# Optimization experiments

Hardware: AMD Instinct MI355X
Metric: run time of the kernel (lower is better)

Reference implementation:

```python
import jax, jax.numpy as jnp
import numpy as np

B, S, D, MULT, K, EPS = 8, 2048, 512, 4, 9, 1e-6


def setup_inputs() -> dict:
    key = jax.random.key(0)
    ks = jax.random.split(key, 12)
    w = lambda k, shape, s=0.02: jax.random.normal(k, shape, dtype=jnp.float32) * s
    return dict(
        x=jax.random.normal(ks[0], (B, S, D), dtype=jnp.float32),
        g=jnp.ones((D,), jnp.float32),
        W1=w(ks[1], (D, D)), b1=jnp.zeros((D,), jnp.float32),
        W2=w(ks[2], (D, D)), b2=jnp.zeros((D,), jnp.float32),
        dw_w=w(ks[3], (D, D, K)), dw_b=jnp.zeros((D,), jnp.float32),
        pw_w=w(ks[4], (D, D, 1)), pw_b=jnp.zeros((D,), jnp.float32),
        Wi=w(ks[5], (D, D)), bi=jnp.zeros((D,), jnp.float32),
        Wr=w(ks[6], (D, D)), br=jnp.zeros((D,), jnp.float32),
        lam=jax.random.normal(ks[7], (D,), dtype=jnp.float32),
        Wm1=w(ks[8], (D, D * MULT)), bm1=jnp.zeros((D * MULT,), jnp.float32),
        Wm2=w(ks[9], (D * MULT, D)), bm2=jnp.zeros((D,), jnp.float32),
    )


def _rglru(x, Wi, bi, Wr, br, lam):
    # Griffin RG-LRU: h_t = a_t * h_{t-1} + sqrt(1 - a_t^2) * (i_t * x_t), h_0 = 0
    r = jax.nn.sigmoid(x @ Wr + br)                 # [B,S,D] recurrence gate
    i = jax.nn.sigmoid(x @ Wi + bi)                 # [B,S,D] input gate
    log_a = -8.0 * jax.nn.softplus(lam) * r         # [B,S,D]
    a = jnp.exp(log_a)
    b = jnp.sqrt(1.0 - jnp.exp(2.0 * log_a)) * (i * x)

    def combine(e1, e2):
        a1, b1 = e1
        a2, b2 = e2
        return (a1 * a2, a2 * b1 + b2)

    _, h = jax.lax.associative_scan(combine, (a, b), axis=1)
    return h


def _conv1d(x_cdS, w_oik, b_o, pad):
    y = jax.lax.conv_general_dilated(
        x_cdS, w_oik, window_strides=(1,), padding=[pad],
        dimension_numbers=("NCH", "OIH", "NCH"))
    return y + b_o[None, :, None]


def reference(x, g, W1, b1, W2, b2, dw_w, dw_b, pw_w, pw_b,
              Wi, bi, Wr, br, lam, Wm1, bm1, Wm2, bm2):
    scale = jnp.sqrt(jnp.float32(D))

    def rms(t):  # matches torch: x / (||x||_2 + eps) * sqrt(D) * g
        n = jnp.linalg.norm(t, axis=-1, keepdims=True) + EPS
        return t / n * scale * g

    skip = x
    xn = rms(x)
    l1 = xn @ W1 + b1                               # [B,S,D]
    l2 = xn @ W2 + b2                               # [B,S,D]
    c = jnp.transpose(l1, (0, 2, 1))                # [B,D,S]
    c = _conv1d(c, dw_w, dw_b, (K // 2, K // 2))    # 'same' padding, k=9
    c = _conv1d(c, pw_w, pw_b, (0, 0))              # pointwise k=1
    l1 = jnp.transpose(c, (0, 2, 1))                # [B,S,D]
    l1 = _rglru(l1, Wi, bi, Wr, br, lam)
    x1 = l1 * jax.nn.gelu(l2, approximate=False) + skip

    skip2 = x1
    xn2 = rms(x1)
    h = xn2 @ Wm1 + bm1                             # [B,S,4D]
    out = (jax.nn.gelu(h, approximate=False) * h) @ Wm2 + bm2 + skip2
    return out
```

## Files before the change

kernel.cpp:

```cpp
#include <hip/hip_runtime.h>
#include <hip/hip_bf16.h>

typedef unsigned short ushort_t;
typedef unsigned short vus8 __attribute__((ext_vector_type(8)));
typedef short vs8 __attribute__((ext_vector_type(8)));
typedef float vf4 __attribute__((ext_vector_type(4)));

#define D_DIM 512
#define S_LEN 2048
#define B_SZ 8
#define T_TOK 16384
#define NCH 64
#define CLEN 32

__device__ __forceinline__ float bf2f(ushort_t u) {
  union { unsigned int i; float f; } v;
  v.i = ((unsigned int)u) << 16;
  return v.f;
}
__device__ __forceinline__ ushort_t f2bf(float f) {
  union { float f; unsigned int i; } v;
  v.f = f;
  unsigned int r = v.i + 0x7fffu + ((v.i >> 16) & 1u);
  return (ushort_t)(r >> 16);
}
__device__ __forceinline__ float gelu_exact(float x) {
  return 0.5f * x * (1.0f + erff(x * 0.7071067811865475f));
}
__device__ __forceinline__ float ld_in(const void* p, size_t i, int fl) {
  return fl ? ((const float*)p)[i] : bf2f(((const ushort_t*)p)[i]);
}
__device__ __forceinline__ int dt_fl(const ushort_t* gdt) {
  return !(gdt[0] == 0x3F80 && gdt[1] == 0x3F80);
}
__device__ __forceinline__ void gld_lds16(const ushort_t* g, ushort_t* l) {
  __builtin_amdgcn_global_load_lds(
      (const __attribute__((address_space(1))) unsigned int*)g,
      (__attribute__((address_space(3))) unsigned int*)l, 16, 0, 0);
}

__device__ __forceinline__ void ab_compute(ushort_t rp, ushort_t ip, ushort_t xv,
                                           float sp8, float& a, float& b) {
  float r = 1.f / (1.f + expf(-bf2f(rp)));
  float ig = 1.f / (1.f + expf(-bf2f(ip)));
  float la = -sp8 * r;
  a = expf(la);
  b = sqrtf(fmaxf(0.f, -expm1f(2.f * la))) * ig * bf2f(xv);
}

#define NJOBS 18
struct PrepJobs {
  const void* src[NJOBS];
  ushort_t* dst[NJOBS];
  int R[NJOBS];
  int C[NJOBS];
  int mode[NJOBS];
  int start[NJOBS];
  const void* gsrc;
  int njobs;
};
__global__ void mega_prep(PrepJobs J, const ushort_t* __restrict__ gdt) {
  __shared__ ushort_t ts[32][33];
  int fl = dt_fl(gdt);
  int bid = blockIdx.x;
  int j = 0;
  while (j + 1 < J.njobs && bid >= J.start[j + 1]) j++;
  int tile = bid - J.start[j];
  const void* in = J.src[j];
  ushort_t* out = J.dst[j];
  int mode = J.mode[j];
  if (mode == 2) {
    int n = J.R[j];
    int base = tile * 8192;
#pragma unroll 4
    for (int q = 0; q < 32; q++) {
      int i = base + q * 256 + threadIdx.x;
      if (i < n) out[i] = fl ? f2bf(((const float*)in)[i]) : ((const ushort_t*)in)[i];
    }
    return;
  }
  int R = J.R[j], C = J.C[j];
  int tpr = C >> 5;
  int bc = tile % tpr, br = tile / tpr;
  int tx = threadIdx.x & 31, ty = threadIdx.x >> 5;
#pragma unroll
  for (int i = 0; i < 32; i += 8) {
    size_t idx = (size_t)(br * 32 + ty + i) * C + bc * 32 + tx;
    ts[ty + i][tx] = fl ? f2bf(((const float*)in)[idx]) : ((const ushort_t*)in)[idx];
  }
  __syncthreads();
#pragma unroll
  for (int i = 0; i < 32; i += 8) {
    int r = bc * 32 + ty + i;
    int orow = (mode == 1) ? (r % 9) * 512 + r / 9 : r;
    ushort_t val = ts[tx][ty + i];
    if (mode == 3) {
      int kcol = br * 32 + tx;
      val = f2bf(bf2f(val) * ld_in(J.gsrc, kcol, fl));
    }
    out[(size_t)orow * R + br * 32 + tx] = val;
  }
}

__global__ void gam_kernel(const ushort_t* __restrict__ tpw, const ushort_t* __restrict__ dwbc,
                           const ushort_t* __restrict__ pwbc, const ushort_t* __restrict__ lamc,
                           float* __restrict__ gam, float* __restrict__ sp8b) {
  int t = blockIdx.x * 256 + threadIdx.x;
  if (t < 512) {
    float l = bf2f(lamc[t]);
    sp8b[t] = 8.f * ((l > 20.f) ? l : log1pf(expf(l)));
  }
  int wave = threadIdx.x >> 6, lane = threadIdx.x & 63;
  int o = blockIdx.x * 4 + wave;
  vus8 v = *(const vus8*)(tpw + (size_t)o * 512 + lane * 8);
  vus8 w = *(const vus8*)(dwbc + lane * 8);
  float p = 0.f;
#pragma unroll
  for (int q = 0; q < 8; q++) p += bf2f(v[q]) * bf2f(w[q]);
#pragma unroll
  for (int off = 32; off; off >>= 1) p += __shfl_xor(p, off, 64);
  if (lane == 0) gam[o] = p + bf2f(pwbc[o]);
}

__global__ void rms_kernel(const void* __restrict__ x, const ushort_t* __restrict__ gdt,
                           const ushort_t* __restrict__ gc, ushort_t* __restrict__ out) {
  int fl = dt_fl(gdt);
  int wave = threadIdx.x >> 6, lane = threadIdx.x & 63;
  int row = blockIdx.x * 4 + wave;
  size_t base = (size_t)row * D_DIM + lane * 8;
  float f[8];
  float ss = 0.f;
#pragma unroll
  for (int j = 0; j < 8; j++) { f[j] = ld_in(x, base + j, fl); ss += f[j] * f[j]; }
#pragma unroll
  for (int off = 32; off > 0; off >>= 1) ss += __shfl_xor(ss, off, 64);
  float sc = 22.62741699796952f / (sqrtf(ss) + 1e-6f);
  vus8 o;
#pragma unroll
  for (int j = 0; j < 8; j++) o[j] = f2bf(f[j] * sc * bf2f(gc[lane * 8 + j]));
  *(vus8*)(out + base) = o;
}

template <int ACT>
__global__ __launch_bounds__(256, 2) void gemm_bt(
    const ushort_t* __restrict__ A, const ushort_t* __restrict__ Bt,
    const ushort_t* __restrict__ bias, void* __restrict__ Cv,
    const ushort_t* __restrict__ skip, const float* __restrict__ rowss,
    const ushort_t* __restrict__ gdt, int N, int K, int lda, int row0,
    size_t zsA, size_t zsB, size_t zsC) {
  __shared__ __align__(16) ushort_t As[128 * 32];
  __shared__ __align__(16) ushort_t Bs[128 * 32];
  A += (size_t)blockIdx.z * zsA;
  Bt += (size_t)blockIdx.z * zsB;
  const size_t zC = (size_t)blockIdx.z * zsC;
  const int tid = threadIdx.x;
  const int bm = blockIdx.y, bn = blockIdx.x;
  const int wave = tid >> 6, lane = tid & 63;
  const int wm = wave & 1, wn = wave >> 1;
  const int quad = lane >> 4, l16 = lane & 15;
  const int ofl = (ACT == 2) ? dt_fl(gdt) : 0;
  const int srow = wave * 32 + (lane >> 2);
  const int scol = (lane & 3) * 8;
  const ushort_t* gA = A + (size_t)(bm * 128 + srow) * lda + scol;
  const ushort_t* gB = Bt + (size_t)(bn * 128 + srow) * K + scol;
  ushort_t* lA0 = As + (wave * 32) * 32;
  ushort_t* lA1 = As + (wave * 32 + 16) * 32;
  ushort_t* lB0 = Bs + (wave * 32) * 32;
  ushort_t* lB1 = Bs + (wave * 32 + 16) * 32;
  vf4 acc[4][4] = {};
  for (int k0 = 0; k0 < K; k0 += 32) {
    __syncthreads();
    gld_lds16(gA + k0, lA0);
    gld_lds16(gA + k0 + (size_t)16 * lda, lA1);
    gld_lds16(gB + k0, lB0);
    gld_lds16(gB + k0 + (size_t)16 * K, lB1);
    __syncthreads();
    vs8 af[4], bfr[4];
#pragma unroll
    for (int mi = 0; mi < 4; mi++)
      af[mi] = *(const vs8*)(As + (wm * 64 + mi * 16 + l16) * 32 + quad * 8);
#pragma unroll
    for (int ni = 0; ni < 4; ni++)
      bfr[ni] = *(const vs8*)(Bs + (wn * 64 + ni * 16 + l16) * 32 + quad * 8);
#pragma unroll
    for (int mi = 0; mi < 4; mi++)
#pragma unroll
      for (int ni = 0; ni < 4; ni++)
        acc[mi][ni] =
            __builtin_amdgcn_mfma_f32_16x16x32_bf16(af[mi], bfr[ni], acc[mi][ni], 0, 0, 0);
  }
#pragma unroll
  for (int mi = 0; mi < 4; mi++) {
#pragma unroll
    for (int ni = 0; ni < 4; ni++) {
      int gcol = bn * 128 + wn * 64 + ni * 16 + l16;
      float bv = bias ? bf2f(bias[gcol]) : 0.f;
#pragma unroll
      for (int r = 0; r < 4; r++) {
        int grow = row0 + bm * 128 + wm * 64 + mi * 16 + quad * 4 + r;
        size_t oidx = zC + (size_t)grow * N + gcol;
        float v;
        if (ACT == 3) {
          float sc = 22.62741699796952f / (sqrtf(rowss[grow]) + 1e-6f);
          v = acc[mi][ni][r] * sc + bv;
          v = gelu_exact(v) * v;
        } else {
          v = acc[mi][ni][r] + bv;
        }
        if (ACT == 2) v += bf2f(skip[(size_t)grow * N + gcol]);
        if (ACT == 2 && ofl) ((float*)Cv)[oidx] = v;
        else ((ushort_t*)Cv)[oidx] = f2bf(v);
      }
    }
  }
}

template <int ACT>
__global__ __launch_bounds__(512, 2) void gemm256(
    const ushort_t* __restrict__ A, const ushort_t* __restrict__ Bt,
    const ushort_t* __restrict__ bias, ushort_t* __restrict__ C,
    const float* __restrict__ rowss, int N, int K) {
  __shared__ __align__(16) ushort_t lds[65536];
  const int tid = threadIdx.x;
  const int bn = blockIdx.x, bm = blockIdx.y;
  const int wave = tid >> 6, lane = tid & 63;
  const int wm = wave & 1, wn = wave >> 1;
  const int quad = lane >> 4, l16 = lane & 15;
  const int NT = K >> 5;

  const int r2 = tid >> 2;
  const int scol = (((tid & 3) ^ ((r2 >> 1) & 3)) << 3);
  const ushort_t* gA0 = A + (size_t)(bm * 256 + r2) * K + scol;
  const ushort_t* gB0 = Bt + (size_t)(bn * 256 + r2) * K + scol;
  const size_t hstep = (size_t)128 * K;
  ushort_t* ldsW = lds + (wave << 9);

  const int cA = ((quad ^ ((l16 >> 1) & 3)) << 3);

  vf4 acc[8][4] = {};

#define STAGE(t, slot)                            \
  do {                                            \
    const ushort_t* ga = gA0 + (t) * 32;          \
    const ushort_t* gb = gB0 + (t) * 32;          \
    ushort_t* d = ldsW + (slot) * 16384;          \
    gld_lds16(ga, d);                             \
    gld_lds16(ga + hstep, d + 4096);              \
    gld_lds16(gb, d + 8192);                      \
    gld_lds16(gb + hstep, d + 12288);             \
  } while (0)

  STAGE(0, 0);
  STAGE(1, 1);

  for (int t = 0; t < NT; ++t) {
    if (t + 1 < NT)
      asm volatile("s_waitcnt vmcnt(4)" ::: "memory");
    else
      asm volatile("s_waitcnt vmcnt(0)" ::: "memory");
    __builtin_amdgcn_s_barrier();
    __builtin_amdgcn_sched_barrier(0);
    if (t + 2 < NT) STAGE(t + 2, (t + 2) & 3);
    const ushort_t* L = lds + (t & 3) * 16384;
    vs8 af[8], bf[4];
#pragma unroll
    for (int mi = 0; mi < 8; mi++)
      af[mi] = *(const vs8*)(L + (wm * 128 + mi * 16 + l16) * 32 + cA);
#pragma unroll
    for (int ni = 0; ni < 4; ni++)
      bf[ni] = *(const vs8*)(L + 8192 + (wn * 64 + ni * 16 + l16) * 32 + cA);
    asm volatile("s_waitcnt lgkmcnt(0)" ::: "memory");
    __builtin_amdgcn_sched_barrier(0);
    __builtin_amdgcn_s_setprio(1);
#pragma unroll
    for (int mi = 0; mi < 8; mi++)
#pragma unroll
      for (int ni = 0; ni < 4; ni++)
        acc[mi][ni] =
            __builtin_amdgcn_mfma_f32_16x16x32_bf16(af[mi], bf[ni], acc[mi][ni], 0, 0, 0);
    __builtin_amdgcn_s_setprio(0);
    __builtin_amdgcn_sched_barrier(0);
  }
#undef STAGE

#pragma unroll
  for (int mi = 0; mi < 8; mi++) {
    const int growb = bm * 256 + wm * 128 + mi * 16 + quad * 4;
    float scv[4];
    if (ACT == 3) {
#pragma unroll
      for (int r = 0; r < 4; r++)
        scv[r] = 22.62741699796952f / (sqrtf(rowss[growb + r]) + 1e-6f);
    }
#pragma unroll
    for (int ni = 0; ni < 4; ni++) {
      const int gcol = bn * 256 + wn * 64 + ni * 16 + l16;
      const float bv = bf2f(bias[gcol]);
#pragma unroll
      for (int r = 0; r < 4; r++) {
        float v = acc[mi][ni][r];
        if (ACT == 3) {
          v = v * scv[r] + bv;
          v = gelu_exact(v) * v;
        } else {
          v += bv;
        }
        C[(size_t)(growb + r) * N + gcol] = f2bf(v);
      }
    }
  }
}

#define LDA_CONV 1024
__global__ __launch_bounds__(256, 2) void conv_gemm(
    const ushort_t* __restrict__ A, const ushort_t* __restrict__ Bt9,
    const float* __restrict__ gam, ushort_t* __restrict__ C) {
  __shared__ __align__(16) ushort_t Ah[136 * 32];
  __shared__ __align__(16) ushort_t Bs[3 * 128 * 32];
  const int tid = threadIdx.x;
  const int bid = blockIdx.x;
  const int xid = bid & 7, cid = bid >> 3;
  const int bn = xid >> 1;
  const int bm = (xid & 1) * 64 + cid;
  const int wave = tid >> 6, lane = tid & 63;
  const int wm = wave & 1, wn = wave >> 1;
  const int quad = lane >> 4, l16 = lane & 15;
  const int pos = bm & 15;
  const bool first = (pos == 0), last = (pos == 15);
  const int blrow = lane >> 2;
  const int bscol = (lane & 3) * 8;
  vf4 acc[4][4] = {};
  for (int k0 = 0; k0 < D_DIM; k0 += 32) {
    __syncthreads();
    for (int c = tid; c < 544; c += 256) {
      int j = c >> 2, col = (c & 3) * 8;
      vus8 v = {0, 0, 0, 0, 0, 0, 0, 0};
      bool valid = !((first && j < 4) || (last && j >= 132));
      if (valid)
        v = *(const vus8*)(A + (size_t)(bm * 128 + j - 4) * LDA_CONV + k0 + col);
      *(vus8*)(Ah + j * 32 + col) = v;
    }
#pragma unroll
    for (int kg = 0; kg < 3; kg++) {
      if (kg) __syncthreads();
#pragma unroll
      for (int h = 0; h < 6; h++) {
        int m = h * 4 + wave;
        int r = m * 16 + blrow;
        int kbl = m >> 3;
        int ro = r & 127;
        const ushort_t* g = Bt9 + ((size_t)(kg * 3 + kbl) * D_DIM + bn * 128 + ro) * D_DIM +
                            k0 + bscol;
        gld_lds16(g, Bs + m * 16 * 32);
      }
      __syncthreads();
#pragma unroll
      for (int kbl = 0; kbl < 3; kbl++) {
        int kb = kg * 3 + kbl;
        vs8 af[4], bfr[4];
#pragma unroll
        for (int mi = 0; mi < 4; mi++)
          af[mi] = *(const vs8*)(Ah + (wm * 64 + mi * 16 + l16 + kb) * 32 + quad * 8);
#pragma unroll
        for (int ni = 0; ni < 4; ni++)
          bfr[ni] = *(const vs8*)(Bs + kbl * 4096 + (wn * 64 + ni * 16 + l16) * 32 + quad * 8);
#pragma unroll
        for (int mi = 0; mi < 4; mi++)
#pragma unroll
          for (int ni = 0; ni < 4; ni++)
            acc[mi][ni] =
                __builtin_amdgcn_mfma_f32_16x16x32_bf16(af[mi], bfr[ni], acc[mi][ni], 0, 0, 0);
      }
    }
  }
#pragma unroll
  for (int mi = 0; mi < 4; mi++) {
#pragma unroll
    for (int ni = 0; ni < 4; ni++) {
      int gcol = bn * 128 + wn * 64 + ni * 16 + l16;
      float gv = gam[gcol];
#pragma unroll
      for (int r = 0; r < 4; r++) {
        int grow = bm * 128 + wm * 64 + mi * 16 + quad * 4 + r;
        C[(size_t)grow * D_DIM + gcol] = f2bf(acc[mi][ni][r] + gv);
      }
    }
  }
}

__global__ void scan_pass1(const ushort_t* __restrict__ P, const ushort_t* __restrict__ xin,
                           const float* __restrict__ sp8b, float* __restrict__ Aagg,
                           float* __restrict__ Bagg) {
  int bid = blockIdx.x;
  int dblk = bid & 1, c = (bid >> 1) & (NCH - 1), bb = bid >> 7;
  int d = dblk * 256 + threadIdx.x;
  float sp8 = sp8b[d];
  size_t baseP = ((size_t)bb * S_LEN + c * CLEN) * 1024 + d;
  size_t baseX = ((size_t)bb * S_LEN + c * CLEN) * D_DIM + d;
  float Ap = 1.f, h = 0.f;
  for (int s = 0; s < CLEN; s++) {
    float av, bv;
    ab_compute(P[baseP + (size_t)s * 1024], P[baseP + 512 + (size_t)s * 1024],
               xin[baseX + (size_t)s * D_DIM], sp8, av, bv);
    Ap *= av;
    h = av * h + bv;
  }
  size_t o = ((size_t)bb * NCH + c) * D_DIM + d;
  Aagg[o] = Ap;
  Bagg[o] = h;
}

__global__ void scan_carry(const float* __restrict__ Aagg, const float* __restrict__ Bagg,
                           float* __restrict__ carry) {
  int idx = blockIdx.x * 256 + threadIdx.x;
  int bb = idx >> 9, d = idx & (D_DIM - 1);
  float h = 0.f;
  for (int c = 0; c < NCH; c++) {
    size_t o = ((size_t)bb * NCH + c) * D_DIM + d;
    carry[o] = h;
    h = Aagg[o] * h + Bagg[o];
  }
}

__global__ void scan_pass2(const ushort_t* __restrict__ P, const float* __restrict__ sp8b,
                           const float* __restrict__ carry, const ushort_t* __restrict__ P12,
                           const void* __restrict__ x, const ushort_t* __restrict__ gdt,
                           ushort_t* xio, float* __restrict__ rowss) {
  int fl = dt_fl(gdt);
  int bid = blockIdx.x;
  int dblk = bid & 1, c = (bid >> 1) & (NCH - 1), bb = bid >> 7;
  int d = dblk * 256 + threadIdx.x;
  int lane = threadIdx.x & 63;
  float sp8 = sp8b[d];
  float h = carry[((size_t)bb * NCH + c) * D_DIM + d];
  size_t baseP = ((size_t)bb * S_LEN + c * CLEN) * 1024 + d;
  size_t baseL = ((size_t)bb * S_LEN + c * CLEN) * 1024 + 512 + d;
  size_t base = ((size_t)bb * S_LEN + c * CLEN) * D_DIM + d;
  int row0 = bb * S_LEN + c * CLEN;
  for (int s = 0; s < CLEN; s++) {
    size_t idx = base + (size_t)s * D_DIM;
    float av, bv;
    ab_compute(P[baseP + (size_t)s * 1024], P[baseP + 512 + (size_t)s * 1024], xio[idx], sp8,
               av, bv);
    h = av * h + bv;
    float l2v = bf2f(P12[baseL + (size_t)s * 1024]);
    float xv = ld_in(x, idx, fl);
    float v = h * gelu_exact(l2v) + xv;
    xio[idx] = f2bf(v);
    float p = v * v;
#pragma unroll
    for (int o2 = 32; o2; o2 >>= 1) p += __shfl_xor(p, o2, 64);
    if (lane == 0) atomicAdd(&rowss[row0 + s], p);
  }
}

extern "C" void kernel_launch(void* const* d_in, const int* in_sizes, int n_in, void* d_out,
                              int out_size, void* d_ws, size_t ws_size, hipStream_t stream) {
  (void)in_sizes; (void)n_in; (void)out_size; (void)ws_size;
  const void* x   = d_in[0];
  const void* g   = d_in[1];
  const void* W1  = d_in[2];
  const void* b1  = d_in[3];
  const void* W2  = d_in[4];
  const void* b2  = d_in[5];
  const void* dww = d_in[6];
  const void* dwb = d_in[7];
  const void* pww = d_in[8];
  const void* pwb = d_in[9];
  const void* Wi  = d_in[10];
  const void* bi  = d_in[11];
  const void* Wr  = d_in[12];
  const void* br  = d_in[13];
  const void* lam = d_in[14];
  const void* Wm1 = d_in[15];
  const void* bm1 = d_in[16];
  const void* Wm2 = d_in[17];
  const void* bm2 = d_in[18];
  const ushort_t* gdt = (const ushort_t*)g;

  char* ws = (char*)d_ws;
  size_t off = 0;
  auto take = [&](size_t n) {
    void* p = ws + off;
    off += (n + 255) & ~(size_t)255;
    return p;
  };
  const size_t ACT_B = (size_t)T_TOK * D_DIM * 2;
  ushort_t* tW12 = (ushort_t*)take((size_t)1024 * 512 * 2);
  ushort_t* tWri = (ushort_t*)take((size_t)1024 * 512 * 2);
  ushort_t* tWm1 = (ushort_t*)take((size_t)2048 * 512 * 2);
  ushort_t* tWm2 = (ushort_t*)take((size_t)2048 * 512 * 2);
  ushort_t* Wp   = (ushort_t*)take((size_t)9 * 512 * 512 * 2);
  ushort_t* gc   = (ushort_t*)take(512 * 2);
  ushort_t* lamc = (ushort_t*)take(512 * 2);
  ushort_t* b12c = (ushort_t*)take(1024 * 2);
  ushort_t* bric = (ushort_t*)take(1024 * 2);
  ushort_t* bm2c = (ushort_t*)take(512 * 2);
  ushort_t* bm1c = (ushort_t*)take(2048 * 2);
  ushort_t* dwbc = (ushort_t*)take(512 * 2);
  ushort_t* pwbc = (ushort_t*)take(512 * 2);
  float* gam     = (float*)take(512 * 4);
  float* sp8b    = (float*)take(512 * 4);
  float* rowss   = (float*)take((size_t)T_TOK * 4);
  ushort_t* S0 = (ushort_t*)take(ACT_B);
  ushort_t* S1 = (ushort_t*)take(ACT_B);
  ushort_t* S2 = (ushort_t*)take(ACT_B);
  ushort_t* S3 = (ushort_t*)take(ACT_B);
  ushort_t* S4 = (ushort_t*)take(ACT_B);
  float* Aagg  = (float*)take((size_t)B_SZ * NCH * D_DIM * 4);
  float* Bagg  = (float*)take((size_t)B_SZ * NCH * D_DIM * 4);
  float* carry = (float*)take((size_t)B_SZ * NCH * D_DIM * 4);
  ushort_t* tpw  = S0;
  ushort_t* tdwT = S1;
  ushort_t* Pri  = S0;
  ushort_t* P12  = S2;
  ushort_t* u    = S0;

  hipMemsetAsync(rowss, 0, (size_t)T_TOK * 4, stream);

  PrepJobs J;
  const void* js[NJOBS] = {g, lam, b1, b2, dwb, pwb, br, bi, bm2, bm1, pww,
                           W1, W2, Wr, Wi, Wm1, Wm2, dww};
  ushort_t* jd[NJOBS] = {gc, lamc, b12c, b12c + 512, dwbc, pwbc, bric, bric + 512, bm2c, bm1c,
                         tpw, tW12, tW12 + (size_t)512 * 512, tWri, tWri + (size_t)512 * 512,
                         tWm1, tWm2, tdwT};
  int jR[NJOBS] = {512, 512, 512, 512, 512, 512, 512, 512, 512, 2048, 262144,
                   512, 512, 512, 512, 512, 2048, 512};
  int jC[NJOBS] = {0, 0, 0, 0, 0, 0, 0, 0, 0, 0, 0, 512, 512, 512, 512, 2048, 512, 4608};
  int jm[NJOBS] = {2, 2, 2, 2, 2, 2, 2, 2, 2, 2, 2, 0, 0, 0, 0, 3, 0, 1};
  int cum = 0;
  for (int i = 0; i < NJOBS; i++) {
    J.src[i] = js[i]; J.dst[i] = jd[i]; J.R[i] = jR[i]; J.C[i] = jC[i]; J.mode[i] = jm[i];
    J.start[i] = cum;
    cum += (jm[i] == 2) ? (jR[i] + 8191) / 8192 : (jC[i] / 32) * (jR[i] / 32);
  }
  J.gsrc = g;
  J.njobs = NJOBS;
  mega_prep<<<cum, 256, 0, stream>>>(J, gdt);
  gemm_bt<0><<<dim3(4, 4, 9), 256, 0, stream>>>(tpw, tdwT, nullptr, Wp, nullptr, nullptr, gdt,
                                                512, 512, 512, 0, 0, (size_t)512 * 512,
                                                (size_t)512 * 512);
  gam_kernel<<<128, 256, 0, stream>>>(tpw, dwbc, pwbc, lamc, gam, sp8b);

  rms_kernel<<<T_TOK / 4, 256, 0, stream>>>(x, gdt, gc, S4);
  gemm256<0><<<dim3(4, 64), 512, 0, stream>>>(S4, tW12, b12c, P12, nullptr, 1024, 512);
  conv_gemm<<<512, 256, 0, stream>>>(P12, Wp, gam, S4);
  gemm256<0><<<dim3(4, 64), 512, 0, stream>>>(S4, tWri, bric, Pri, nullptr, 1024, 512);
  scan_pass1<<<B_SZ * NCH * 2, 256, 0, stream>>>(Pri, S4, sp8b, Aagg, Bagg);
  scan_carry<<<16, 256, 0, stream>>>(Aagg, Bagg, carry);
  scan_pass2<<<B_SZ * NCH * 2, 256, 0, stream>>>(Pri, sp8b, carry, P12, x, gdt, S4, rowss);

  gemm256<3><<<dim3(8, 64), 512, 0, stream>>>(S4, tWm1, bm1c, u, rowss, 2048, 512);
  gemm_bt<2><<<dim3(4, 128), 256, 0, stream>>>(u, tWm2, bm2c, d_out, S4, nullptr, gdt, 512,
                                               2048, 2048, 0, 0, 0, 0);
}
```

Baseline: 509.5 us.

## Rewrite conv GEMM as pipelined 256-row kernel over zero-padded activation buffer

The W1/W2 GEMM now writes its output into a buffer that has 16 zero-padded rows per batch, so the depthwise+pointwise conv GEMM can read halo rows without boundary checks. Zeroing of the pad rows is added to the prep kernel. The conv kernel is replaced by a 512-thread, 256-row-tile version that software-pipelines global-to-LDS async loads of A (double buffered) and B (4 slots) across the 9 taps. It uses swizzled LDS layouts, explicit waitcnt and barriers, and raised priority around the MFMA blocks. The aim is to hide load latency and cut LDS bank conflicts, at the cost of fragile hand-tuned waitcnt counts and more LDS per block.

New measurement: 526.9 us. 3.4% more time.

```diff
diff --git a/kernel.cpp b/kernel.cpp
--- a/kernel.cpp
+++ b/kernel.cpp
@@ -12,6 +12,7 @@
 #define T_TOK 16384
 #define NCH 64
 #define CLEN 32
+#define APAD_ROWS 16640
 
 __device__ __forceinline__ float bf2f(ushort_t u) {
   union { unsigned int i; float f; } v;
@@ -48,7 +49,7 @@
   b = sqrtf(fmaxf(0.f, -expm1f(2.f * la))) * ig * bf2f(xv);
 }
 
-#define NJOBS 18
+#define NJOBS 27
 struct PrepJobs {
   const void* src[NJOBS];
   ushort_t* dst[NJOBS];
@@ -69,13 +70,15 @@
   const void* in = J.src[j];
   ushort_t* out = J.dst[j];
   int mode = J.mode[j];
-  if (mode == 2) {
+  if (mode == 2 || mode == 4) {
     int n = J.R[j];
     int base = tile * 8192;
 #pragma unroll 4
     for (int q = 0; q < 32; q++) {
       int i = base + q * 256 + threadIdx.x;
-      if (i < n) out[i] = fl ? f2bf(((const float*)in)[i]) : ((const ushort_t*)in)[i];
+      if (i < n)
+        out[i] = (mode == 4) ? (ushort_t)0
+                             : (fl ? f2bf(((const float*)in)[i]) : ((const ushort_t*)in)[i]);
     }
     return;
   }
@@ -305,83 +308,116 @@
         } else {
           v += bv;
         }
-        C[(size_t)(growb + r) * N + gcol] = f2bf(v);
+        int grow = growb + r;
+        size_t orow = (ACT == 1) ? (size_t)grow + (size_t)((grow >> 11) << 4) + 4
+                                 : (size_t)grow;
+        C[orow * N + gcol] = f2bf(v);
       }
     }
   }
 }
 
-#define LDA_CONV 1024
-__global__ __launch_bounds__(256, 2) void conv_gemm(
-    const ushort_t* __restrict__ A, const ushort_t* __restrict__ Bt9,
+__global__ __launch_bounds__(512, 2) void conv256(
+    const ushort_t* __restrict__ Apad, const ushort_t* __restrict__ Wp,
     const float* __restrict__ gam, ushort_t* __restrict__ C) {
-  __shared__ __align__(16) ushort_t Ah[136 * 32];
-  __shared__ __align__(16) ushort_t Bs[3 * 128 * 32];
+  __shared__ __align__(16) ushort_t Asl[2 * 12288];
+  __shared__ __align__(16) ushort_t Bsl[4 * 4096];
   const int tid = threadIdx.x;
-  const int bid = blockIdx.x;
-  const int xid = bid & 7, cid = bid >> 3;
-  const int bn = xid >> 1;
-  const int bm = (xid & 1) * 64 + cid;
+  const int bn = blockIdx.x;
+  const int bmg = blockIdx.y;
+  const int batch = bmg >> 3, seg = bmg & 7;
   const int wave = tid >> 6, lane = tid & 63;
-  const int wm = wave & 1, wn = wave >> 1;
+  const int wm = wave >> 1, wn = wave & 1;
   const int quad = lane >> 4, l16 = lane & 15;
-  const int pos = bm & 15;
-  const bool first = (pos == 0), last = (pos == 15);
-  const int blrow = lane >> 2;
-  const int bscol = (lane & 3) * 8;
+  const int r2 = tid >> 2;
+  const int sw0 = (((tid & 3) ^ ((r2 >> 1) & 3)) << 3);
+  const int cB = ((quad ^ ((l16 >> 1) & 3)) << 3);
+  const int bnc = bn * 128;
+  const size_t tb = (size_t)batch * 2064 + seg * 256;
+  const ushort_t* A0 = Apad + tb * 1024;
+
   vf4 acc[4][4] = {};
-  for (int k0 = 0; k0 < D_DIM; k0 += 32) {
-    __syncthreads();
-    for (int c = tid; c < 544; c += 256) {
-      int j = c >> 2, col = (c & 3) * 8;
-      vus8 v = {0, 0, 0, 0, 0, 0, 0, 0};
-      bool valid = !((first && j < 4) || (last && j >= 132));
-      if (valid)
-        v = *(const vus8*)(A + (size_t)(bm * 128 + j - 4) * LDA_CONV + k0 + col);
-      *(vus8*)(Ah + j * 32 + col) = v;
-    }
-#pragma unroll
-    for (int kg = 0; kg < 3; kg++) {
-      if (kg) __syncthreads();
-#pragma unroll
-      for (int h = 0; h < 6; h++) {
-        int m = h * 4 + wave;
-        int r = m * 16 + blrow;
-        int kbl = m >> 3;
-        int ro = r & 127;
-        const ushort_t* g = Bt9 + ((size_t)(kg * 3 + kbl) * D_DIM + bn * 128 + ro) * D_DIM +
-                            k0 + bscol;
-        gld_lds16(g, Bs + m * 16 * 32);
-      }
-      __syncthreads();
-#pragma unroll
-      for (int kbl = 0; kbl < 3; kbl++) {
-        int kb = kg * 3 + kbl;
-        vs8 af[4], bfr[4];
-#pragma unroll
-        for (int mi = 0; mi < 4; mi++)
-          af[mi] = *(const vs8*)(Ah + (wm * 64 + mi * 16 + l16 + kb) * 32 + quad * 8);
-#pragma unroll
-        for (int ni = 0; ni < 4; ni++)
-          bfr[ni] = *(const vs8*)(Bs + kbl * 4096 + (wn * 64 + ni * 16 + l16) * 32 + quad * 8);
-#pragma unroll
-        for (int mi = 0; mi < 4; mi++)
-#pragma unroll
-          for (int ni = 0; ni < 4; ni++)
-            acc[mi][ni] =
-                __builtin_amdgcn_mfma_f32_16x16x32_bf16(af[mi], bfr[ni], acc[mi][ni], 0, 0, 0);
-      }
-    }
-  }
+
+  auto stageA = [&](int tt, int slot, int part) {
+    gld_lds16(A0 + (size_t)(part * 128 + r2) * 1024 + tt * 32 + sw0,
+              Asl + slot * 12288 + part * 4096 + wave * 512);
+  };
+  auto stageB = [&](int tt, int pp, int slot) {
+    gld_lds16(Wp + (size_t)(pp * 512 + bnc + r2) * 512 + tt * 32 + sw0,
+              Bsl + slot * 4096 + wave * 512);
+  };
+
+#define CPHASE(T, P, NSTR, DO_A, DO_B)                                            \
+  do {                                                                            \
+    asm volatile("s_waitcnt " NSTR ::: "memory");                                 \
+    __builtin_amdgcn_s_barrier();                                                 \
+    __builtin_amdgcn_sched_barrier(0);                                            \
+    if (DO_A) stageA((T) + 1, ((T) + 1) & 1, (P));                                \
+    if (DO_B) {                                                                   \
+      int pp = (P) + 2, tt = (T);                                                 \
+      if (pp >= 9) { pp -= 9; tt++; }                                             \
+      stageB(tt, pp, ((T) * 9 + (P) + 2) & 3);                                    \
+    }                                                                             \
+    const ushort_t* LA = Asl + ((T) & 1) * 12288;                                 \
+    const ushort_t* LB = Bsl + (((T) * 9 + (P)) & 3) * 4096;                      \
+    vs8 af[4], bfv[4];                                                            \
+    _Pragma("unroll") for (int mi = 0; mi < 4; mi++) {                            \
+      int row = wm * 64 + mi * 16 + l16 + (P);                                    \
+      af[mi] = *(const vs8*)(LA + row * 32 + ((quad ^ ((row >> 1) & 3)) << 3));   \
+    }                                                                             \
+    _Pragma("unroll") for (int ni = 0; ni < 4; ni++)                              \
+      bfv[ni] = *(const vs8*)(LB + (wn * 64 + ni * 16 + l16) * 32 + cB);          \
+    asm volatile("s_waitcnt lgkmcnt(0)" ::: "memory");                            \
+    __builtin_amdgcn_sched_barrier(0);                                            \
+    __builtin_amdgcn_s_setprio(1);                                                \
+    _Pragma("unroll") for (int mi = 0; mi < 4; mi++)                              \
+      _Pragma("unroll") for (int ni = 0; ni < 4; ni++)                            \
+        acc[mi][ni] = __builtin_amdgcn_mfma_f32_16x16x32_bf16(af[mi], bfv[ni],    \
+                                                              acc[mi][ni], 0, 0, 0); \
+    __builtin_amdgcn_s_setprio(0);                                                \
+    __builtin_amdgcn_sched_barrier(0);                                            \
+  } while (0)
+
+  stageA(0, 0, 0);
+  stageA(0, 0, 1);
+  stageA(0, 0, 2);
+  stageB(0, 0, 0);
+  stageB(0, 1, 1);
+
+  for (int t = 0; t < 15; ++t) {
+    CPHASE(t, 0, "vmcnt(1)", 1, 1);
+    CPHASE(t, 1, "vmcnt(2)", 1, 1);
+    CPHASE(t, 2, "vmcnt(2)", 1, 1);
+    CPHASE(t, 3, "vmcnt(2)", 0, 1);
+    CPHASE(t, 4, "vmcnt(1)", 0, 1);
+    CPHASE(t, 5, "vmcnt(1)", 0, 1);
+    CPHASE(t, 6, "vmcnt(1)", 0, 1);
+    CPHASE(t, 7, "vmcnt(1)", 0, 1);
+    CPHASE(t, 8, "vmcnt(1)", 0, 1);
+  }
+  {
+    const int t = 15;
+    CPHASE(t, 0, "vmcnt(0)", 0, 1);
+    CPHASE(t, 1, "vmcnt(0)", 0, 1);
+    CPHASE(t, 2, "vmcnt(0)", 0, 1);
+    CPHASE(t, 3, "vmcnt(0)", 0, 1);
+    CPHASE(t, 4, "vmcnt(0)", 0, 1);
+    CPHASE(t, 5, "vmcnt(0)", 0, 1);
+    CPHASE(t, 6, "vmcnt(0)", 0, 1);
+    CPHASE(t, 7, "vmcnt(0)", 0, 0);
+    CPHASE(t, 8, "vmcnt(0)", 0, 0);
+  }
+#undef CPHASE
+
 #pragma unroll
   for (int mi = 0; mi < 4; mi++) {
 #pragma unroll
     for (int ni = 0; ni < 4; ni++) {
-      int gcol = bn * 128 + wn * 64 + ni * 16 + l16;
+      int gcol = bnc + wn * 64 + ni * 16 + l16;
       float gv = gam[gcol];
 #pragma unroll
       for (int r = 0; r < 4; r++) {
-        int grow = bm * 128 + wm * 64 + mi * 16 + quad * 4 + r;
+        int grow = (batch << 11) + seg * 256 + wm * 64 + mi * 16 + quad * 4 + r;
         C[(size_t)grow * D_DIM + gcol] = f2bf(acc[mi][ni][r] + gv);
       }
     }
@@ -423,7 +459,7 @@
 }
 
 __global__ void scan_pass2(const ushort_t* __restrict__ P, const float* __restrict__ sp8b,
-                           const float* __restrict__ carry, const ushort_t* __restrict__ P12,
+                           const float* __restrict__ carry, const ushort_t* __restrict__ l2p,
                            const void* __restrict__ x, const ushort_t* __restrict__ gdt,
                            ushort_t* xio, float* __restrict__ rowss) {
   int fl = dt_fl(gdt);
@@ -434,7 +470,7 @@
   float sp8 = sp8b[d];
   float h = carry[((size_t)bb * NCH + c) * D_DIM + d];
   size_t baseP = ((size_t)bb * S_LEN + c * CLEN) * 1024 + d;
-  size_t baseL = ((size_t)bb * S_LEN + c * CLEN) * 1024 + 512 + d;
+  size_t baseL = ((size_t)bb * 2064 + 4 + c * CLEN) * 1024 + 512 + d;
   size_t base = ((size_t)bb * S_LEN + c * CLEN) * D_DIM + d;
   int row0 = bb * S_LEN + c * CLEN;
   for (int s = 0; s < CLEN; s++) {
@@ -443,7 +479,7 @@
     ab_compute(P[baseP + (size_t)s * 1024], P[baseP + 512 + (size_t)s * 1024], xio[idx], sp8,
                av, bv);
     h = av * h + bv;
-    float l2v = bf2f(P12[baseL + (size_t)s * 1024]);
+    float l2v = bf2f(l2p[baseL + (size_t)s * 1024]);
     float xv = ld_in(x, idx, fl);
     float v = h * gelu_exact(l2v) + xv;
     xio[idx] = f2bf(v);
@@ -502,37 +538,47 @@
   float* gam     = (float*)take(512 * 4);
   float* sp8b    = (float*)take(512 * 4);
   float* rowss   = (float*)take((size_t)T_TOK * 4);
-  ushort_t* S0 = (ushort_t*)take(ACT_B);
-  ushort_t* S1 = (ushort_t*)take(ACT_B);
-  ushort_t* S2 = (ushort_t*)take(ACT_B);
-  ushort_t* S3 = (ushort_t*)take(ACT_B);
-  ushort_t* S4 = (ushort_t*)take(ACT_B);
+  ushort_t* Apad2 = (ushort_t*)take((size_t)APAD_ROWS * 1024 * 2);
+  ushort_t* PriB  = (ushort_t*)take((size_t)T_TOK * 1024 * 2);
+  ushort_t* S4    = (ushort_t*)take(ACT_B);
   float* Aagg  = (float*)take((size_t)B_SZ * NCH * D_DIM * 4);
   float* Bagg  = (float*)take((size_t)B_SZ * NCH * D_DIM * 4);
   float* carry = (float*)take((size_t)B_SZ * NCH * D_DIM * 4);
-  ushort_t* tpw  = S0;
-  ushort_t* tdwT = S1;
-  ushort_t* Pri  = S0;
-  ushort_t* P12  = S2;
-  ushort_t* u    = S0;
+  ushort_t* tpw  = PriB;
+  ushort_t* tdwT = PriB + 262144;
+  ushort_t* u    = Apad2;
 
   hipMemsetAsync(rowss, 0, (size_t)T_TOK * 4, stream);
 
   PrepJobs J;
   const void* js[NJOBS] = {g, lam, b1, b2, dwb, pwb, br, bi, bm2, bm1, pww,
-                           W1, W2, Wr, Wi, Wm1, Wm2, dww};
+                           W1, W2, Wr, Wi, Wm1, Wm2, dww,
+                           nullptr, nullptr, nullptr, nullptr, nullptr, nullptr, nullptr,
+                           nullptr, nullptr};
   ushort_t* jd[NJOBS] = {gc, lamc, b12c, b12c + 512, dwbc, pwbc, bric, bric + 512, bm2c, bm1c,
                          tpw, tW12, tW12 + (size_t)512 * 512, tWri, tWri + (size_t)512 * 512,
-                         tWm1, tWm2, tdwT};
+                         tWm1, tWm2, tdwT,
+                         Apad2,
+                         Apad2 + (size_t)(0 * 2064 + 2052) * 1024,
+                         Apad2 + (size_t)(1 * 2064 + 2052) * 1024,
+                         Apad2 + (size_t)(2 * 2064 + 2052) * 1024,
+                         Apad2 + (size_t)(3 * 2064 + 2052) * 1024,
+                         Apad2 + (size_t)(4 * 2064 + 2052) * 1024,
+                         Apad2 + (size_t)(5 * 2064 + 2052) * 1024,
+                         Apad2 + (size_t)(6 * 2064 + 2052) * 1024,
+                         Apad2 + (size_t)(7 * 2064 + 2052) * 1024};
   int jR[NJOBS] = {512, 512, 512, 512, 512, 512, 512, 512, 512, 2048, 262144,
-                   512, 512, 512, 512, 512, 2048, 512};
-  int jC[NJOBS] = {0, 0, 0, 0, 0, 0, 0, 0, 0, 0, 0, 512, 512, 512, 512, 2048, 512, 4608};
-  int jm[NJOBS] = {2, 2, 2, 2, 2, 2, 2, 2, 2, 2, 2, 0, 0, 0, 0, 3, 0, 1};
+                   512, 512, 512, 512, 512, 2048, 512,
+                   4096, 16384, 16384, 16384, 16384, 16384, 16384, 16384, 12288};
+  int jC[NJOBS] = {0, 0, 0, 0, 0, 0, 0, 0, 0, 0, 0, 512, 512, 512, 512, 2048, 512, 4608,
+                   0, 0, 0, 0, 0, 0, 0, 0, 0};
+  int jm[NJOBS] = {2, 2, 2, 2, 2, 2, 2, 2, 2, 2, 2, 0, 0, 0, 0, 3, 0, 1,
+                   4, 4, 4, 4, 4, 4, 4, 4, 4};
   int cum = 0;
   for (int i = 0; i < NJOBS; i++) {
     J.src[i] = js[i]; J.dst[i] = jd[i]; J.R[i] = jR[i]; J.C[i] = jC[i]; J.mode[i] = jm[i];
     J.start[i] = cum;
-    cum += (jm[i] == 2) ? (jR[i] + 8191) / 8192 : (jC[i] / 32) * (jR[i] / 32);
+    cum += (jm[i] == 2 || jm[i] == 4) ? (jR[i] + 8191) / 8192 : (jC[i] / 32) * (jR[i] / 32);
   }
   J.gsrc = g;
   J.njobs = NJOBS;
@@ -543,12 +589,12 @@
   gam_kernel<<<128, 256, 0, stream>>>(tpw, dwbc, pwbc, lamc, gam, sp8b);
 
   rms_kernel<<<T_TOK / 4, 256, 0, stream>>>(x, gdt, gc, S4);
-  gemm256<0><<<dim3(4, 64), 512, 0, stream>>>(S4, tW12, b12c, P12, nullptr, 1024, 512);
-  conv_gemm<<<512, 256, 0, stream>>>(P12, Wp, gam, S4);
-  gemm256<0><<<dim3(4, 64), 512, 0, stream>>>(S4, tWri, bric, Pri, nullptr, 1024, 512);
-  scan_pass1<<<B_SZ * NCH * 2, 256, 0, stream>>>(Pri, S4, sp8b, Aagg, Bagg);
+  gemm256<1><<<dim3(4, 64), 512, 0, stream>>>(S4, tW12, b12c, Apad2, nullptr, 1024, 512);
+  conv256<<<dim3(4, 64), 512, 0, stream>>>(Apad2, Wp, gam, S4);
+  gemm256<0><<<dim3(4, 64), 512, 0, stream>>>(S4, tWri, bric, PriB, nullptr, 1024, 512);
+  scan_pass1<<<B_SZ * NCH * 2, 256, 0, stream>>>(PriB, S4, sp8b, Aagg, Bagg);
   scan_carry<<<16, 256, 0, stream>>>(Aagg, Bagg, carry);
-  scan_pass2<<<B_SZ * NCH * 2, 256, 0, stream>>>(Pri, sp8b, carry, P12, x, gdt, S4, rowss);
+  scan_pass2<<<B_SZ * NCH * 2, 256, 0, stream>>>(PriB, sp8b, carry, Apad2, x, gdt, S4, rowss);
 
   gemm256<3><<<dim3(8, 64), 512, 0, stream>>>(S4, tWm1, bm1c, u, rowss, 2048, 512);
   gemm_bt<2><<<dim3(4, 128), 256, 0, stream>>>(u, tWm2, bm2c, d_out, S4, nullptr, gdt, 512,
```
